# Optimization experiments

Measured on AMD Instinct MI355X. Metric: run time of the kernel, lower is better.

The kernel has to match this reference:

```python
import jax, jax.numpy as jnp
import numpy as np
from jax import lax

B, H, W = 8, 64, 64
C = 192          # in_channel == out_channel
CI = 384         # inner_channel = int(2.0 * C)


def setup_inputs() -> dict:
    key = jax.random.key(0)
    ks = jax.random.split(key, 8)
    s = 0.02
    return {
        "x": jax.random.normal(ks[0], (B, H, W, C), jnp.float32),
        "Win": jax.random.normal(ks[1], (C, 2 * CI), jnp.float32) * s,
        "conv_w": jax.random.normal(ks[2], (CI, 1, 3, 3), jnp.float32) * s,
        "conv_b": jnp.zeros((CI,), jnp.float32),
        "Wout": jax.random.normal(ks[3], (CI, C), jnp.float32) * s,
        "Wm1": jax.random.normal(ks[4], (C, 4 * C), jnp.float32) * s,
        "bm1": jnp.zeros((4 * C,), jnp.float32),
        "Wm2": jax.random.normal(ks[5], (4 * C, C), jnp.float32) * s,
        "bm2": jnp.zeros((C,), jnp.float32),
    }


def reference(x, Win, conv_w, conv_b, Wout, Wm1, bm1, Wm2, bm2):
    silu = jax.nn.silu
    shortcut = x                                   # [B,H,W,C], norm1 is Identity (norm=None)
    xz = jnp.einsum('bhwc,cd->bhwd', x, Win)       # in_proj (no bias) -> [B,H,W,2*CI]
    x1, z = jnp.split(xz, 2, axis=-1)
    # channel_recover -> [B,CI,H,W], depthwise conv + silu
    xc = jnp.transpose(x1, (0, 3, 1, 2))
    xc = lax.conv_general_dilated(xc, conv_w, (1, 1), 'SAME',
                                  feature_group_count=CI,
                                  dimension_numbers=('NCHW', 'OIHW', 'NCHW'))
    xc = silu(xc + conv_b[None, :, None, None])
    L = H * W
    # cross_scan: K=2 views (row-major and transposed), doubled by flip_scan -> [B,4,CI,L]
    x0 = xc.reshape(B, CI, L)
    xt = jnp.transpose(xc, (0, 1, 3, 2)).reshape(B, CI, L)
    x_cross = jnp.stack([x0, xt], axis=1)
    xs = jnp.concatenate([x_cross, jnp.flip(x_cross, axis=-1)], axis=1)
    out_y = xs  # ssm() is abstract in MBaseBlock -> identity passthrough
    # scan_proj (CrossMerge): undo flips and permutations, sum branches
    inv_y = jnp.flip(out_y[:, 2:4], axis=-1)

    def unperm(v):  # branch scanned in transposed (W,H) order -> back to (H,W)
        return jnp.transpose(v.reshape(B, CI, W, H), (0, 1, 3, 2)).reshape(B, CI, L)

    y = out_y[:, 0] + inv_y[:, 0] + unperm(out_y[:, 1]) + unperm(inv_y[:, 1])
    y = jnp.transpose(y, (0, 2, 1)).reshape(B, H, W, CI)  # norm2 is Identity
    y = y * silu(z)                                       # gate
    out = jnp.einsum('bhwc,cd->bhwd', y, Wout)            # out_proj (no bias)
    out = shortcut + out                                  # dropout/drop_path are Identity
    # dense is Identity (in_channel == out_channel); MLP branch 192->768->192
    h = silu(jnp.einsum('bhwc,cd->bhwd', out, Wm1) + bm1)
    mlp = jnp.einsum('bhwd,dc->bhwc', h, Wm2) + bm2
    return out + mlp
```

## Files before the change

kernel.cpp:

```cpp
#include <hip/hip_runtime.h>
#include <hip/hip_bf16.h>

#define BDIM 8
#define HDIM 64
#define WDIM 64
#define CDIM 192
#define CIDIM 384
#define MTOK (BDIM * HDIM * WDIM)

using bf16 = __hip_bfloat16;
typedef __attribute__((ext_vector_type(8))) short short8;
typedef __attribute__((ext_vector_type(4))) float f32x4;

__device__ __forceinline__ float silu_f(float v) { return v / (1.0f + __expf(-v)); }
__device__ __forceinline__ float bf2f(short s) {
    union { unsigned u; float f; } x; x.u = ((unsigned)(unsigned short)s) << 16; return x.f;
}

__device__ __forceinline__ void gload_lds16(const bf16* g, bf16* l) {
    __builtin_amdgcn_global_load_lds(
        (const __attribute__((address_space(1))) void*)g,
        (__attribute__((address_space(3))) void*)l, 16, 0, 0);
}

template <int EPI>
__launch_bounds__(256, 3)
__global__ void gemm_k192(const bf16* __restrict__ A, const bf16* __restrict__ BT,
                          const float* __restrict__ bias,
                          bf16* __restrict__ outB, bf16* __restrict__ outB2,
                          int N, int NX)
{
    __shared__ bf16 As[64 * 192];
    __shared__ bf16 Bs[64 * 192];

    const int bid = blockIdx.x;
    const int c8  = bid & 7;
    const int kk_ = bid >> 3;
    const int bx  = kk_ % NX;
    const int by  = (kk_ / NX) * 8 + c8;
    const int m0  = by * 64;
    const int n0  = bx * 64;

    const int tid  = threadIdx.x;
    const int lane = tid & 63;
    const int wv   = tid >> 6;
    const int wm   = wv >> 1;
    const int wn   = wv & 1;

    #pragma unroll
    for (int i = 0; i < 6; ++i) {
        const int ci   = wv * 6 + i;
        const int c    = ci * 64 + lane;
        const int row  = c / 24;
        const int slot = c - row * 24;
        const int lsl  = slot ^ (row & 7);
        gload_lds16(A  + (size_t)(m0 + row) * 192 + lsl * 8, &As[ci * 512]);
        gload_lds16(BT + (size_t)(n0 + row) * 192 + lsl * 8, &Bs[ci * 512]);
    }
    __syncthreads();

    f32x4 acc[2][2] = {};
    #pragma unroll
    for (int ks = 0; ks < 6; ++ks) {
        const int t = ks * 4 + (lane >> 4);
        short8 af[2], bfr[2];
        #pragma unroll
        for (int mi = 0; mi < 2; ++mi) {
            const int m = wm * 32 + mi * 16 + (lane & 15);
            af[mi] = *reinterpret_cast<const short8*>(&As[m * 192 + ((t ^ (m & 7)) << 3)]);
        }
        #pragma unroll
        for (int ni = 0; ni < 2; ++ni) {
            const int n = wn * 32 + ni * 16 + (lane & 15);
            bfr[ni] = *reinterpret_cast<const short8*>(&Bs[n * 192 + ((t ^ (n & 7)) << 3)]);
        }
        #pragma unroll
        for (int mi = 0; mi < 2; ++mi)
            #pragma unroll
            for (int ni = 0; ni < 2; ++ni)
                acc[mi][ni] = __builtin_amdgcn_mfma_f32_16x16x32_bf16(
                    af[mi], bfr[ni], acc[mi][ni], 0, 0, 0);
    }

    const int colb = n0 + wn * 32 + (lane & 15);
    const int rowb = m0 + wm * 32 + (lane >> 4) * 4;
    #pragma unroll
    for (int mi = 0; mi < 2; ++mi) {
        #pragma unroll
        for (int ni = 0; ni < 2; ++ni) {
            const int c = colb + ni * 16;
            #pragma unroll
            for (int j = 0; j < 4; ++j) {
                const int row = rowb + mi * 16 + j;
                const float v = acc[mi][ni][j];
                if constexpr (EPI == 0) {
                    if (c < CIDIM)
                        outB[(size_t)row * CIDIM + c] = __float2bfloat16(v);
                    else
                        outB2[(size_t)row * CIDIM + (c - CIDIM)] =
                            __float2bfloat16(4.0f * silu_f(v));
                } else {
                    outB[(size_t)row * N + c] = __float2bfloat16(silu_f(v + bias[c]));
                }
            }
        }
    }
}

template <int EPI>
__launch_bounds__(256, 4)
__global__ void gemm_mfma(const bf16* __restrict__ A, const bf16* __restrict__ BT,
                          const float* __restrict__ bias,
                          const float* __restrict__ residF,
                          const bf16* __restrict__ residB,
                          float* __restrict__ outF, bf16* __restrict__ outB,
                          int M, int N, int K, int NX)
{
    __shared__ bf16 As[128 * 64];
    __shared__ bf16 Bs[64 * 64];

    const int bid = blockIdx.x;
    const int c8  = bid & 7;
    const int kq  = bid >> 3;
    const int bx  = kq % NX;
    const int by  = (kq / NX) * 8 + c8;
    const int m0  = by * 128;
    const int n0  = bx * 64;

    const int tid  = threadIdx.x;
    const int lane = tid & 63;
    const int wv   = tid >> 6;
    const int wm   = wv >> 1;
    const int wn   = wv & 1;

    const int srow  = lane >> 3;
    const int sslot = lane & 7;

    f32x4 acc[4][2] = {};

    for (int k0 = 0; k0 < K; k0 += 64) {
        #pragma unroll
        for (int i = 0; i < 4; ++i) {
            const int rb = wv * 32 + i * 8;
            const int r  = rb + srow;
            gload_lds16(A + (size_t)(m0 + r) * K + k0 + ((sslot ^ (r & 7)) << 3),
                        &As[rb * 64]);
        }
        #pragma unroll
        for (int i = 0; i < 2; ++i) {
            const int rb = wv * 16 + i * 8;
            const int r  = rb + srow;
            gload_lds16(BT + (size_t)(n0 + r) * K + k0 + ((sslot ^ (r & 7)) << 3),
                        &Bs[rb * 64]);
        }
        __syncthreads();

        #pragma unroll
        for (int kk = 0; kk < 2; ++kk) {
            const int t = kk * 4 + (lane >> 4);
            short8 af[4], bfr[2];
            #pragma unroll
            for (int mi = 0; mi < 4; ++mi) {
                const int m = wm * 64 + mi * 16 + (lane & 15);
                af[mi] = *reinterpret_cast<const short8*>(&As[m * 64 + ((t ^ (m & 7)) << 3)]);
            }
            #pragma unroll
            for (int ni = 0; ni < 2; ++ni) {
                const int n = wn * 32 + ni * 16 + (lane & 15);
                bfr[ni] = *reinterpret_cast<const short8*>(&Bs[n * 64 + ((t ^ (n & 7)) << 3)]);
            }
            #pragma unroll
            for (int mi = 0; mi < 4; ++mi)
                #pragma unroll
                for (int ni = 0; ni < 2; ++ni)
                    acc[mi][ni] = __builtin_amdgcn_mfma_f32_16x16x32_bf16(
                        af[mi], bfr[ni], acc[mi][ni], 0, 0, 0);
        }
        __syncthreads();
    }

    const int colb = n0 + wn * 32 + (lane & 15);
    const int rowb = m0 + wm * 64 + (lane >> 4) * 4;
    #pragma unroll
    for (int mi = 0; mi < 4; ++mi) {
        #pragma unroll
        for (int ni = 0; ni < 2; ++ni) {
            const int c = colb + ni * 16;
            #pragma unroll
            for (int j = 0; j < 4; ++j) {
                const int row = rowb + mi * 16 + j;
                const size_t off = (size_t)row * N + c;
                const float v = acc[mi][ni][j];
                if constexpr (EPI == 1) {
                    outB[off] = __float2bfloat16(v + residF[off]);
                } else {
                    outF[off] = v + bias[c] + bf2f(*(const short*)&residB[off]);
                }
            }
        }
    }
}

__launch_bounds__(256)
__global__ void dwconv_gate_v6(const bf16* __restrict__ x1, const bf16* __restrict__ sz,
                               const float* __restrict__ wT, const float* __restrict__ conv_b,
                               bf16* __restrict__ y)
{
    const int bid = blockIdx.x;
    const int swz = (bid & 7) * ((int)gridDim.x >> 3) + (bid >> 3);
    const int f   = swz * 256 + threadIdx.x;
    const int m   = f / 48;
    const int cg  = f - m * 48;
    const int c0  = cg * 8;
    const int h   = (m >> 6) & 63;
    const int w   = m & 63;

    float acc[8];
    {
        const f32x4 ba = *reinterpret_cast<const f32x4*>(&conv_b[c0]);
        const f32x4 bb = *reinterpret_cast<const f32x4*>(&conv_b[c0 + 4]);
        acc[0] = ba[0]; acc[1] = ba[1]; acc[2] = ba[2]; acc[3] = ba[3];
        acc[4] = bb[0]; acc[5] = bb[1]; acc[6] = bb[2]; acc[7] = bb[3];
    }

    #pragma unroll
    for (int r = 0; r < 3; ++r) {
        const int hh = h + r - 1;
        if (hh < 0 || hh >= HDIM) continue;
        #pragma unroll
        for (int dw = 0; dw < 3; ++dw) {
            const int ww = w + dw - 1;
            if (ww < 0 || ww >= WDIM) continue;
            const int mm  = m + (r - 1) * WDIM + (dw - 1);
            const int tap = r * 3 + dw;
            const short8 t = *reinterpret_cast<const short8*>(&x1[(size_t)mm * CIDIM + c0]);
            const f32x4 wa = *reinterpret_cast<const f32x4*>(&wT[tap * CIDIM + c0]);
            const f32x4 wb = *reinterpret_cast<const f32x4*>(&wT[tap * CIDIM + c0 + 4]);
            acc[0] += bf2f(t[0]) * wa[0]; acc[1] += bf2f(t[1]) * wa[1];
            acc[2] += bf2f(t[2]) * wa[2]; acc[3] += bf2f(t[3]) * wa[3];
            acc[4] += bf2f(t[4]) * wb[0]; acc[5] += bf2f(t[5]) * wb[1];
            acc[6] += bf2f(t[6]) * wb[2]; acc[7] += bf2f(t[7]) * wb[3];
        }
    }

    const short8 g = *reinterpret_cast<const short8*>(&sz[(size_t)m * CIDIM + c0]);
    bf16 tmp[8];
    #pragma unroll
    for (int j = 0; j < 8; ++j)
        tmp[j] = __float2bfloat16(silu_f(acc[j]) * bf2f(g[j]));
    *reinterpret_cast<short8*>(&y[(size_t)m * CIDIM + c0]) =
        *reinterpret_cast<const short8*>(tmp);
}

#define SZ_WIN  (192 * 768)
#define SZ_WOUT (384 * 192)
#define SZ_WM1  (192 * 768)
#define SZ_WM2  (768 * 192)
#define SZ_CW   (CIDIM * 9)
#define XCVT    (MTOK * CDIM / 4)
#define SZ_ALL  (XCVT + SZ_WIN + SZ_WOUT + SZ_WM1 + SZ_WM2 + SZ_CW)

__launch_bounds__(256)
__global__ void prep_all(const float* __restrict__ x, const float* __restrict__ Win,
                         const float* __restrict__ Wout, const float* __restrict__ Wm1,
                         const float* __restrict__ Wm2, const float* __restrict__ convw,
                         bf16* __restrict__ xb, bf16* __restrict__ WinT,
                         bf16* __restrict__ WoutT, bf16* __restrict__ Wm1T,
                         bf16* __restrict__ Wm2T, float* __restrict__ wTc)
{
    int idx = blockIdx.x * 256 + threadIdx.x;
    if (idx < XCVT) {
        const int i = idx * 4;
        const float4 v = *reinterpret_cast<const float4*>(&x[i]);
        xb[i + 0] = __float2bfloat16(v.x);
        xb[i + 1] = __float2bfloat16(v.y);
        xb[i + 2] = __float2bfloat16(v.z);
        xb[i + 3] = __float2bfloat16(v.w);
        return;
    }
    idx -= XCVT;
    if (idx < SZ_WIN) {
        const int r = idx / 768, c = idx % 768;
        WinT[(size_t)c * 192 + r] = __float2bfloat16(Win[idx]);
        return;
    }
    idx -= SZ_WIN;
    if (idx < SZ_WOUT) {
        const int r = idx / 192, c = idx % 192;
        WoutT[(size_t)c * 384 + r] = __float2bfloat16(Wout[idx]);
        return;
    }
    idx -= SZ_WOUT;
    if (idx < SZ_WM1) {
        const int r = idx / 768, c = idx % 768;
        Wm1T[(size_t)c * 192 + r] = __float2bfloat16(Wm1[idx]);
        return;
    }
    idx -= SZ_WM1;
    if (idx < SZ_WM2) {
        const int r = idx / 192, c = idx % 192;
        Wm2T[(size_t)c * 768 + r] = __float2bfloat16(Wm2[idx]);
        return;
    }
    idx -= SZ_WM2;
    if (idx < SZ_CW) {
        const int ci = idx / 9, t = idx % 9;
        wTc[t * CIDIM + ci] = convw[idx];
    }
}

extern "C" void kernel_launch(void* const* d_in, const int* in_sizes, int n_in,
                              void* d_out, int out_size, void* d_ws, size_t ws_size,
                              hipStream_t stream)
{
    const float* x      = (const float*)d_in[0];
    const float* Win    = (const float*)d_in[1];
    const float* conv_w = (const float*)d_in[2];
    const float* conv_b = (const float*)d_in[3];
    const float* Wout   = (const float*)d_in[4];
    const float* Wm1    = (const float*)d_in[5];
    const float* bm1    = (const float*)d_in[6];
    const float* Wm2    = (const float*)d_in[7];
    const float* bm2    = (const float*)d_in[8];
    float* out = (float*)d_out;

    char* ws = (char*)d_ws;
    size_t o = 0;
    bf16*  xb    = (bf16*)(ws + o); o += (size_t)MTOK * CDIM * 2;
    bf16*  WinT  = (bf16*)(ws + o); o += (size_t)768 * 192 * 2;
    bf16*  WoutT = (bf16*)(ws + o); o += (size_t)192 * 384 * 2;
    bf16*  Wm1T  = (bf16*)(ws + o); o += (size_t)768 * 192 * 2;
    bf16*  Wm2T  = (bf16*)(ws + o); o += (size_t)192 * 768 * 2;
    float* wTc   = (float*)(ws + o); o += (size_t)9 * CIDIM * 4;
    bf16*  ws_x1 = (bf16*)(ws + o); o += (size_t)MTOK * CIDIM * 2;
    bf16*  ws_sz = (bf16*)(ws + o); o += (size_t)MTOK * CIDIM * 2;
    bf16*  ws_y  = (bf16*)(ws + o); o += (size_t)MTOK * CIDIM * 2;
    bf16*  ws_ob = (bf16*)(ws + o); o += (size_t)MTOK * CDIM * 2;
    bf16*  ws_h  = ws_x1;

    prep_all<<<dim3((SZ_ALL + 255) / 256), dim3(256), 0, stream>>>(
        x, Win, Wout, Wm1, Wm2, conv_w, xb, WinT, WoutT, Wm1T, Wm2T, wTc);

    gemm_k192<0><<<dim3(12 * 512), dim3(256), 0, stream>>>(
        xb, WinT, nullptr, ws_x1, ws_sz, 768, 12);

    dwconv_gate_v6<<<dim3(MTOK * 48 / 256), dim3(256), 0, stream>>>(
        ws_x1, ws_sz, wTc, conv_b, ws_y);

    gemm_mfma<1><<<dim3(3 * 256), dim3(256), 0, stream>>>(
        ws_y, WoutT, nullptr, x, nullptr, nullptr, ws_ob, MTOK, CDIM, CIDIM, 3);

    gemm_k192<2><<<dim3(12 * 512), dim3(256), 0, stream>>>(
        ws_ob, Wm1T, bm1, ws_h, nullptr, 768, 12);

    gemm_mfma<3><<<dim3(3 * 256), dim3(256), 0, stream>>>(
        ws_h, Wm2T, bm2, nullptr, ws_ob, out, nullptr, MTOK, CDIM, 768, 3);
}
```

Before: 124.1 us.

## Make K=192 GEMMs persistent with resident B tile and double-buffered A

Replaces the one-tile-per-block K=192 GEMM with a persistent kernel. Each block keeps one 64-column B tile resident in LDS and walks a stripe of M tiles, prefetching the next A tile into a second LDS buffer while it computes the current one. This removes repeated B loads and the per-block launch and prologue cost, and hides global load latency. In exchange the grid shrinks to 480 blocks with more LDS per block (occupancy 2), and there is a barrier after every tile.

Result: no change. 121.8 us (-1.8%).

```diff
diff --git a/kernel.cpp b/kernel.cpp
--- a/kernel.cpp
+++ b/kernel.cpp
@@ -23,23 +23,20 @@
         (__attribute__((address_space(3))) void*)l, 16, 0, 0);
 }
 
+#define NSTRIPE 40
 template <int EPI>
-__launch_bounds__(256, 3)
-__global__ void gemm_k192(const bf16* __restrict__ A, const bf16* __restrict__ BT,
-                          const float* __restrict__ bias,
-                          bf16* __restrict__ outB, bf16* __restrict__ outB2,
-                          int N, int NX)
-{
-    __shared__ bf16 As[64 * 192];
+__launch_bounds__(256, 2)
+__global__ void gemm_k192_p(const bf16* __restrict__ A, const bf16* __restrict__ BT,
+                            const float* __restrict__ bias,
+                            bf16* __restrict__ outB, bf16* __restrict__ outB2)
+{
+    __shared__ bf16 As[2][64 * 192];
     __shared__ bf16 Bs[64 * 192];
 
     const int bid = blockIdx.x;
-    const int c8  = bid & 7;
-    const int kk_ = bid >> 3;
-    const int bx  = kk_ % NX;
-    const int by  = (kk_ / NX) * 8 + c8;
-    const int m0  = by * 64;
-    const int n0  = bx * 64;
+    const int n   = bid / NSTRIPE;
+    const int s   = bid % NSTRIPE;
+    const int n0  = n * 64;
 
     const int tid  = threadIdx.x;
     const int lane = tid & 63;
@@ -47,6 +44,7 @@
     const int wm   = wv >> 1;
     const int wn   = wv & 1;
 
+    int soff[6];
     #pragma unroll
     for (int i = 0; i < 6; ++i) {
         const int ci   = wv * 6 + i;
@@ -54,56 +52,84 @@
         const int row  = c / 24;
         const int slot = c - row * 24;
         const int lsl  = slot ^ (row & 7);
-        gload_lds16(A  + (size_t)(m0 + row) * 192 + lsl * 8, &As[ci * 512]);
-        gload_lds16(BT + (size_t)(n0 + row) * 192 + lsl * 8, &Bs[ci * 512]);
-    }
+        soff[i] = row * 192 + lsl * 8;
+    }
+
+    #pragma unroll
+    for (int i = 0; i < 6; ++i)
+        gload_lds16(BT + (size_t)n0 * 192 + soff[i], &Bs[(wv * 6 + i) * 512]);
+
+    #pragma unroll
+    for (int i = 0; i < 6; ++i)
+        gload_lds16(A + (size_t)(s * 64) * 192 + soff[i], &As[0][(wv * 6 + i) * 512]);
     __syncthreads();
 
-    f32x4 acc[2][2] = {};
-    #pragma unroll
-    for (int ks = 0; ks < 6; ++ks) {
-        const int t = ks * 4 + (lane >> 4);
-        short8 af[2], bfr[2];
+    const int mloc[2] = { wm * 32 + (lane & 15), wm * 32 + 16 + (lane & 15) };
+    const int nloc[2] = { wn * 32 + (lane & 15), wn * 32 + 16 + (lane & 15) };
+    const bool isZ = (EPI == 0) && (n0 >= CIDIM);
+    bf16* dst        = (EPI == 0) ? (isZ ? outB2 : outB) : outB;
+    const int stride = (EPI == 0) ? CIDIM : 768;
+    const int col0   = (EPI == 0) ? (isZ ? n0 - CIDIM : n0) : n0;
+
+    int cur = 0;
+    for (int mt = s; mt < 512; mt += NSTRIPE) {
+        const int nmt = mt + NSTRIPE;
+        if (nmt < 512) {
+            const bf16* a1 = A + (size_t)(nmt * 64) * 192;
+            bf16* db = As[cur ^ 1];
+            #pragma unroll
+            for (int i = 0; i < 6; ++i)
+                gload_lds16(a1 + soff[i], &db[(wv * 6 + i) * 512]);
+        }
+
+        const bf16* la = As[cur];
+        f32x4 acc[2][2] = {};
+        #pragma unroll
+        for (int ks = 0; ks < 6; ++ks) {
+            const int t = ks * 4 + (lane >> 4);
+            short8 af[2], bfr[2];
+            #pragma unroll
+            for (int mi = 0; mi < 2; ++mi) {
+                const int m = mloc[mi];
+                af[mi] = *reinterpret_cast<const short8*>(&la[m * 192 + ((t ^ (m & 7)) << 3)]);
+            }
+            #pragma unroll
+            for (int ni = 0; ni < 2; ++ni) {
+                const int nn = nloc[ni];
+                bfr[ni] = *reinterpret_cast<const short8*>(&Bs[nn * 192 + ((t ^ (nn & 7)) << 3)]);
+            }
+            #pragma unroll
+            for (int mi = 0; mi < 2; ++mi)
+                #pragma unroll
+                for (int ni = 0; ni < 2; ++ni)
+                    acc[mi][ni] = __builtin_amdgcn_mfma_f32_16x16x32_bf16(
+                        af[mi], bfr[ni], acc[mi][ni], 0, 0, 0);
+        }
+
+        const int m0   = mt * 64;
+        const int rowb = m0 + wm * 32 + (lane >> 4) * 4;
+        const int colb = col0 + wn * 32 + (lane & 15);
         #pragma unroll
         for (int mi = 0; mi < 2; ++mi) {
-            const int m = wm * 32 + mi * 16 + (lane & 15);
-            af[mi] = *reinterpret_cast<const short8*>(&As[m * 192 + ((t ^ (m & 7)) << 3)]);
-        }
-        #pragma unroll
-        for (int ni = 0; ni < 2; ++ni) {
-            const int n = wn * 32 + ni * 16 + (lane & 15);
-            bfr[ni] = *reinterpret_cast<const short8*>(&Bs[n * 192 + ((t ^ (n & 7)) << 3)]);
-        }
-        #pragma unroll
-        for (int mi = 0; mi < 2; ++mi)
-            #pragma unroll
-            for (int ni = 0; ni < 2; ++ni)
-                acc[mi][ni] = __builtin_amdgcn_mfma_f32_16x16x32_bf16(
-                    af[mi], bfr[ni], acc[mi][ni], 0, 0, 0);
-    }
-
-    const int colb = n0 + wn * 32 + (lane & 15);
-    const int rowb = m0 + wm * 32 + (lane >> 4) * 4;
-    #pragma unroll
-    for (int mi = 0; mi < 2; ++mi) {
-        #pragma unroll
-        for (int ni = 0; ni < 2; ++ni) {
-            const int c = colb + ni * 16;
-            #pragma unroll
-            for (int j = 0; j < 4; ++j) {
-                const int row = rowb + mi * 16 + j;
-                const float v = acc[mi][ni][j];
-                if constexpr (EPI == 0) {
-                    if (c < CIDIM)
-                        outB[(size_t)row * CIDIM + c] = __float2bfloat16(v);
-                    else
-                        outB2[(size_t)row * CIDIM + (c - CIDIM)] =
-                            __float2bfloat16(4.0f * silu_f(v));
-                } else {
-                    outB[(size_t)row * N + c] = __float2bfloat16(silu_f(v + bias[c]));
+            #pragma unroll
+            for (int ni = 0; ni < 2; ++ni) {
+                const int c = colb + ni * 16;
+                #pragma unroll
+                for (int j = 0; j < 4; ++j) {
+                    const int row = rowb + mi * 16 + j;
+                    float v = acc[mi][ni][j];
+                    if constexpr (EPI == 0) {
+                        if (isZ) v = 4.0f * silu_f(v);
+                    } else {
+                        v = silu_f(v + bias[n0 + (c - col0)]);
+                    }
+                    dst[(size_t)row * stride + c] = __float2bfloat16(v);
                 }
             }
         }
+
+        __syncthreads();
+        cur ^= 1;
     }
 }
 
@@ -341,8 +367,8 @@
     prep_all<<<dim3((SZ_ALL + 255) / 256), dim3(256), 0, stream>>>(
         x, Win, Wout, Wm1, Wm2, conv_w, xb, WinT, WoutT, Wm1T, Wm2T, wTc);
 
-    gemm_k192<0><<<dim3(12 * 512), dim3(256), 0, stream>>>(
-        xb, WinT, nullptr, ws_x1, ws_sz, 768, 12);
+    gemm_k192_p<0><<<dim3(12 * NSTRIPE), dim3(256), 0, stream>>>(
+        xb, WinT, nullptr, ws_x1, ws_sz);
 
     dwconv_gate_v6<<<dim3(MTOK * 48 / 256), dim3(256), 0, stream>>>(
         ws_x1, ws_sz, wTc, conv_b, ws_y);
@@ -350,8 +376,8 @@
     gemm_mfma<1><<<dim3(3 * 256), dim3(256), 0, stream>>>(
         ws_y, WoutT, nullptr, x, nullptr, nullptr, ws_ob, MTOK, CDIM, CIDIM, 3);
 
-    gemm_k192<2><<<dim3(12 * 512), dim3(256), 0, stream>>>(
-        ws_ob, Wm1T, bm1, ws_h, nullptr, 768, 12);
+    gemm_k192_p<2><<<dim3(12 * NSTRIPE), dim3(256), 0, stream>>>(
+        ws_ob, Wm1T, bm1, ws_h, nullptr);
 
     gemm_mfma<3><<<dim3(3 * 256), dim3(256), 0, stream>>>(
         ws_h, Wm2T, bm2, nullptr, ws_ob, out, nullptr, MTOK, CDIM, 768, 3);
```

## Load K=192 GEMM operands directly into registers, bypassing LDS

Applied to the files above, without the earlier changes.

Replaces the LDS-staged K=192 GEMM with a version where each wave reads its A and B MFMA fragments straight from global memory into registers. This removes the shared-memory fill and the barrier, and raises the occupancy hint from 3 to 4. Block-to-tile mapping also changes so each XCD gets a contiguous range of tiles, which should improve L2 locality. In exchange, each A row is fetched by both wn waves and each B tile by both wm waves, and the per-lane 16-byte loads are strided, so global/L2 traffic and load efficiency may get worse.

New measurement: 212.1 us. 1.71x slower.

```diff
diff --git a/kernel.cpp b/kernel.cpp
--- a/kernel.cpp
+++ b/kernel.cpp
@@ -24,66 +24,57 @@
 }
 
 template <int EPI>
-__launch_bounds__(256, 3)
-__global__ void gemm_k192(const bf16* __restrict__ A, const bf16* __restrict__ BT,
-                          const float* __restrict__ bias,
-                          bf16* __restrict__ outB, bf16* __restrict__ outB2,
-                          int N, int NX)
-{
-    __shared__ bf16 As[64 * 192];
-    __shared__ bf16 Bs[64 * 192];
-
+__launch_bounds__(256, 4)
+__global__ void gemm_k192_reg(const bf16* __restrict__ A, const bf16* __restrict__ BT,
+                              const float* __restrict__ bias,
+                              bf16* __restrict__ outB, bf16* __restrict__ outB2)
+{
     const int bid = blockIdx.x;
-    const int c8  = bid & 7;
-    const int kk_ = bid >> 3;
-    const int bx  = kk_ % NX;
-    const int by  = (kk_ / NX) * 8 + c8;
-    const int m0  = by * 64;
-    const int n0  = bx * 64;
-
-    const int tid  = threadIdx.x;
-    const int lane = tid & 63;
-    const int wv   = tid >> 6;
+    const int xcd = bid & 7;
+    const int idx = bid >> 3;
+    const int t   = xcd * 768 + idx;
+    const int mt  = t / 12;
+    const int nt  = t - mt * 12;
+    const int m0  = mt * 64;
+    const int n0  = nt * 64;
+
+    const int lane = threadIdx.x & 63;
+    const int wv   = threadIdx.x >> 6;
     const int wm   = wv >> 1;
     const int wn   = wv & 1;
-
-    #pragma unroll
-    for (int i = 0; i < 6; ++i) {
-        const int ci   = wv * 6 + i;
-        const int c    = ci * 64 + lane;
-        const int row  = c / 24;
-        const int slot = c - row * 24;
-        const int lsl  = slot ^ (row & 7);
-        gload_lds16(A  + (size_t)(m0 + row) * 192 + lsl * 8, &As[ci * 512]);
-        gload_lds16(BT + (size_t)(n0 + row) * 192 + lsl * 8, &Bs[ci * 512]);
-    }
-    __syncthreads();
+    const int l15  = lane & 15;
+    const int l4   = lane >> 4;
+
+    short8 bfr[2][6];
+    #pragma unroll
+    for (int ni = 0; ni < 2; ++ni) {
+        const bf16* bp = BT + (size_t)(n0 + wn * 32 + ni * 16 + l15) * 192 + l4 * 8;
+        #pragma unroll
+        for (int ks = 0; ks < 6; ++ks)
+            bfr[ni][ks] = *reinterpret_cast<const short8*>(bp + ks * 32);
+    }
+
+    const bf16* ap0 = A + (size_t)(m0 + wm * 32 + l15) * 192 + l4 * 8;
+    const bf16* ap1 = A + (size_t)(m0 + wm * 32 + 16 + l15) * 192 + l4 * 8;
 
     f32x4 acc[2][2] = {};
     #pragma unroll
     for (int ks = 0; ks < 6; ++ks) {
-        const int t = ks * 4 + (lane >> 4);
-        short8 af[2], bfr[2];
-        #pragma unroll
-        for (int mi = 0; mi < 2; ++mi) {
-            const int m = wm * 32 + mi * 16 + (lane & 15);
-            af[mi] = *reinterpret_cast<const short8*>(&As[m * 192 + ((t ^ (m & 7)) << 3)]);
-        }
-        #pragma unroll
-        for (int ni = 0; ni < 2; ++ni) {
-            const int n = wn * 32 + ni * 16 + (lane & 15);
-            bfr[ni] = *reinterpret_cast<const short8*>(&Bs[n * 192 + ((t ^ (n & 7)) << 3)]);
-        }
-        #pragma unroll
-        for (int mi = 0; mi < 2; ++mi)
-            #pragma unroll
-            for (int ni = 0; ni < 2; ++ni)
-                acc[mi][ni] = __builtin_amdgcn_mfma_f32_16x16x32_bf16(
-                    af[mi], bfr[ni], acc[mi][ni], 0, 0, 0);
-    }
-
-    const int colb = n0 + wn * 32 + (lane & 15);
-    const int rowb = m0 + wm * 32 + (lane >> 4) * 4;
+        const short8 a0 = *reinterpret_cast<const short8*>(ap0 + ks * 32);
+        const short8 a1 = *reinterpret_cast<const short8*>(ap1 + ks * 32);
+        acc[0][0] = __builtin_amdgcn_mfma_f32_16x16x32_bf16(a0, bfr[0][ks], acc[0][0], 0, 0, 0);
+        acc[0][1] = __builtin_amdgcn_mfma_f32_16x16x32_bf16(a0, bfr[1][ks], acc[0][1], 0, 0, 0);
+        acc[1][0] = __builtin_amdgcn_mfma_f32_16x16x32_bf16(a1, bfr[0][ks], acc[1][0], 0, 0, 0);
+        acc[1][1] = __builtin_amdgcn_mfma_f32_16x16x32_bf16(a1, bfr[1][ks], acc[1][1], 0, 0, 0);
+    }
+
+    const bool isZ   = (EPI == 0) && (n0 >= CIDIM);
+    bf16* dst        = (EPI == 0) ? (isZ ? outB2 : outB) : outB;
+    const int stride = (EPI == 0) ? CIDIM : 768;
+    const int col0   = (EPI == 0) ? (isZ ? n0 - CIDIM : n0) : n0;
+
+    const int rowb = m0 + wm * 32 + l4 * 4;
+    const int colb = col0 + wn * 32 + l15;
     #pragma unroll
     for (int mi = 0; mi < 2; ++mi) {
         #pragma unroll
@@ -92,16 +83,13 @@
             #pragma unroll
             for (int j = 0; j < 4; ++j) {
                 const int row = rowb + mi * 16 + j;
-                const float v = acc[mi][ni][j];
+                float v = acc[mi][ni][j];
                 if constexpr (EPI == 0) {
-                    if (c < CIDIM)
-                        outB[(size_t)row * CIDIM + c] = __float2bfloat16(v);
-                    else
-                        outB2[(size_t)row * CIDIM + (c - CIDIM)] =
-                            __float2bfloat16(4.0f * silu_f(v));
+                    if (isZ) v = 4.0f * silu_f(v);
                 } else {
-                    outB[(size_t)row * N + c] = __float2bfloat16(silu_f(v + bias[c]));
+                    v = silu_f(v + bias[n0 + (c - col0)]);
                 }
+                dst[(size_t)row * stride + c] = __float2bfloat16(v);
             }
         }
     }
@@ -341,8 +329,8 @@
     prep_all<<<dim3((SZ_ALL + 255) / 256), dim3(256), 0, stream>>>(
         x, Win, Wout, Wm1, Wm2, conv_w, xb, WinT, WoutT, Wm1T, Wm2T, wTc);
 
-    gemm_k192<0><<<dim3(12 * 512), dim3(256), 0, stream>>>(
-        xb, WinT, nullptr, ws_x1, ws_sz, 768, 12);
+    gemm_k192_reg<0><<<dim3(512 * 12), dim3(256), 0, stream>>>(
+        xb, WinT, nullptr, ws_x1, ws_sz);
 
     dwconv_gate_v6<<<dim3(MTOK * 48 / 256), dim3(256), 0, stream>>>(
         ws_x1, ws_sz, wTc, conv_b, ws_y);
@@ -350,8 +338,8 @@
     gemm_mfma<1><<<dim3(3 * 256), dim3(256), 0, stream>>>(
         ws_y, WoutT, nullptr, x, nullptr, nullptr, ws_ob, MTOK, CDIM, CIDIM, 3);
 
-    gemm_k192<2><<<dim3(12 * 512), dim3(256), 0, stream>>>(
-        ws_ob, Wm1T, bm1, ws_h, nullptr, 768, 12);
+    gemm_k192_reg<2><<<dim3(512 * 12), dim3(256), 0, stream>>>(
+        ws_ob, Wm1T, bm1, ws_h, nullptr);
 
     gemm_mfma<3><<<dim3(3 * 256), dim3(256), 0, stream>>>(
         ws_h, Wm2T, bm2, nullptr, ws_ob, out, nullptr, MTOK, CDIM, 768, 3);
```
